# Optimization experiments

Hardware: AMD Instinct MI355X
Metric: run time of the kernel (lower is better)

The kernel has to match this reference:

```python
import jax, jax.numpy as jnp
import numpy as np

N_NODES = 50000
N_EDGES = 800000
NUM_IN, NUM_HID, NUM_OUT = 512, 256, 64
EPS = 1e-12


def agnn_conv(x, src, dst, beta, num_nodes):
    # PyG AGNNConv: score(j->i) = beta * cos(x_i, x_j); softmax over incoming
    # edges of each target node i; out_i = sum_j alpha_ij * x_j.
    norm = jnp.maximum(jnp.linalg.norm(x, axis=1, keepdims=True), EPS)
    xn = x / norm                                      # [N, H]
    scores = beta * jnp.sum(xn[dst] * xn[src], axis=1)  # [E]
    m = jax.ops.segment_max(scores, dst, num_segments=num_nodes)
    e = jnp.exp(scores - m[dst])
    s = jax.ops.segment_sum(e, dst, num_segments=num_nodes)
    alpha = e / s[dst]                                  # [E]
    return jax.ops.segment_sum(alpha[:, None] * x[src], dst, num_segments=num_nodes)


def setup_inputs() -> dict:
    key = jax.random.key(0)
    ks = jax.random.split(key, 7)
    x = jax.random.normal(ks[0], (N_NODES, NUM_IN), dtype=jnp.float32)
    edge_index = jax.random.randint(ks[1], (2, N_EDGES), 0, N_NODES, dtype=jnp.int64)
    w1 = jax.random.normal(ks[2], (NUM_HID, NUM_IN), dtype=jnp.float32) / np.sqrt(NUM_IN)
    b1 = jnp.zeros((NUM_HID,), dtype=jnp.float32)
    beta2 = jnp.ones((1,), dtype=jnp.float32)
    w2 = jax.random.normal(ks[3], (NUM_OUT, NUM_HID), dtype=jnp.float32) / np.sqrt(NUM_HID)
    b2 = jnp.zeros((NUM_OUT,), dtype=jnp.float32)
    return {"x": x, "edge_index": edge_index, "w1": w1, "b1": b1,
            "beta2": beta2, "w2": w2, "b2": b2}


def reference(x, edge_index, w1, b1, beta2, w2, b2):
    n = x.shape[0]
    # add self-loops (PyG AGNNConv default add_self_loops=True)
    loops = jnp.arange(n, dtype=edge_index.dtype)
    src = jnp.concatenate([edge_index[0], loops])
    dst = jnp.concatenate([edge_index[1], loops])

    h = jax.nn.relu(x @ w1.T + b1)                       # [N, H] (eval: dropout = id)
    h = agnn_conv(h, src, dst, jnp.float32(1.0), n)      # prop1, fixed beta=1
    z1 = h
    h = agnn_conv(h, src, dst, beta2[0], n)              # prop2, learnable beta
    z2 = h
    logits = h @ w2.T + b2                               # [N, C]
    return (z1, z2, jax.nn.log_softmax(logits, axis=1))
```

## Files before the change

kernel.cpp:

```cpp
#include <hip/hip_runtime.h>

#define N_NODES 50000
#define N_EDGES 800000
#define ETOT (N_EDGES + N_NODES)
#define DIN 512
#define HID 256
#define NOUT 64
#define SCAN_CHUNK 2048

typedef __attribute__((ext_vector_type(8))) short short8;
typedef __attribute__((ext_vector_type(4))) float f32x4;
typedef __attribute__((ext_vector_type(4))) unsigned short us4;

__device__ __forceinline__ unsigned short f2bf(float f) {
  union { float f; unsigned u; } x; x.f = f;
  unsigned r = x.u + 0x7fff + ((x.u >> 16) & 1);
  return (unsigned short)(r >> 16);
}
__device__ __forceinline__ float bf2f(unsigned short b) {
  return __uint_as_float(((unsigned)b) << 16);
}

__device__ __forceinline__ int edge_at(const void* ei, long long idx, int is32) {
  if (is32) return ((const int*)ei)[idx];
  return (int)((const long long*)ei)[idx];
}

__global__ void initK(const void* ei, int* cursor, int* flag) {
  int i = blockIdx.x * blockDim.x + threadIdx.x;
  if (i < N_NODES) cursor[i] = 1;
  if (blockIdx.x == 0 && threadIdx.x < 64) {
    int lane = threadIdx.x;
    bool bad = false;
#pragma unroll
    for (int j = 0; j < 32; ++j) {
      long long v = ((const long long*)ei)[lane * 32 + j];
      bad |= (v < 0 || v >= N_NODES);
    }
    bool anybad = __any(bad);
    if (lane == 0) *flag = anybad ? 1 : 0;
  }
}

__global__ void histK(const void* ei, const int* flag, int* cursor) {
  int e = blockIdx.x * blockDim.x + threadIdx.x;
  if (e >= N_EDGES) return;
  int f = *flag;
  int d = edge_at(ei, (long long)N_EDGES + e, f);
  atomicAdd(&cursor[d], 1);
}

__global__ void scan1K(const int* counts, int* excl, int* bsums) {
  __shared__ int sdata[256];
  int base = blockIdx.x * SCAN_CHUNK;
  int t = threadIdx.x;
  int local[8];
  int sum = 0;
#pragma unroll
  for (int j = 0; j < 8; ++j) {
    int idx = base + t * 8 + j;
    int v = (idx < N_NODES) ? counts[idx] : 0;
    local[j] = sum;
    sum += v;
  }
  sdata[t] = sum;
  __syncthreads();
  for (int off = 1; off < 256; off <<= 1) {
    int v = (t >= off) ? sdata[t - off] : 0;
    __syncthreads();
    sdata[t] += v;
    __syncthreads();
  }
  int texcl = (t == 0) ? 0 : sdata[t - 1];
#pragma unroll
  for (int j = 0; j < 8; ++j) {
    int idx = base + t * 8 + j;
    if (idx < N_NODES) excl[idx] = texcl + local[j];
  }
  if (t == 255) bsums[blockIdx.x] = sdata[255];
}

__global__ void scan2K(int* bsums, int nb) {
  if (threadIdx.x == 0 && blockIdx.x == 0) {
    int run = 0;
    for (int i = 0; i < nb; ++i) { int v = bsums[i]; bsums[i] = run; run += v; }
  }
}

__global__ void scan3K(int* row_ptr, const int* bsums, int* cursor) {
  int i = blockIdx.x * blockDim.x + threadIdx.x;
  if (i < N_NODES) {
    int v = row_ptr[i] + bsums[i >> 11];
    row_ptr[i] = v;
    cursor[i] = v;
    if (i == 0) row_ptr[N_NODES] = ETOT;
  }
}

__global__ void scatterK(const void* ei, const int* flag, int* cursor, int* col) {
  int e = blockIdx.x * blockDim.x + threadIdx.x;
  if (e < N_EDGES) {
    int f = *flag;
    int s = edge_at(ei, e, f);
    int d = edge_at(ei, (long long)N_EDGES + e, f);
    int pos = atomicAdd(&cursor[d], 1);
    col[pos] = s;
  } else if (e < N_EDGES + N_NODES) {
    int i = e - N_EDGES;
    int pos = atomicAdd(&cursor[i], 1);
    col[pos] = i;
  }
}

__global__ __launch_bounds__(256) void gemm1MF(const float* __restrict__ A,
                                               const float* __restrict__ W,
                                               const float* __restrict__ bias,
                                               unsigned short* __restrict__ C) {
  __shared__ short As[128 * 64];
  __shared__ short Bs[128 * 64];
  int t = threadIdx.x;
  int w = t >> 6, lane = t & 63;
  int wr = w >> 1, wc = w & 1;
  int row0 = blockIdx.x * 128;
  int col0 = blockIdx.y * 128;
  f32x4 acc[4][4];
#pragma unroll
  for (int mi = 0; mi < 4; ++mi)
#pragma unroll
    for (int ni = 0; ni < 4; ++ni) acc[mi][ni] = (f32x4){0.f, 0.f, 0.f, 0.f};

  for (int k0 = 0; k0 < DIN; k0 += 64) {
#pragma unroll
    for (int it = 0; it < 4; ++it) {
      int si = it * 256 + t;
      int r = si >> 3, g = si & 7;
      int slot = g ^ (r & 7);
      int gr = row0 + r;
      gr = (gr < N_NODES) ? gr : (N_NODES - 1);
      const float* pa = &A[(long long)gr * DIN + k0 + g * 8];
      float4 a0 = *(const float4*)pa;
      float4 a1 = *(const float4*)(pa + 4);
      short8 sa;
      sa[0] = f2bf(a0.x); sa[1] = f2bf(a0.y); sa[2] = f2bf(a0.z); sa[3] = f2bf(a0.w);
      sa[4] = f2bf(a1.x); sa[5] = f2bf(a1.y); sa[6] = f2bf(a1.z); sa[7] = f2bf(a1.w);
      *(short8*)&As[(r * 8 + slot) * 8] = sa;
      const float* pb = &W[(long long)(col0 + r) * DIN + k0 + g * 8];
      float4 b0 = *(const float4*)pb;
      float4 b1v = *(const float4*)(pb + 4);
      short8 sb;
      sb[0] = f2bf(b0.x); sb[1] = f2bf(b0.y); sb[2] = f2bf(b0.z); sb[3] = f2bf(b0.w);
      sb[4] = f2bf(b1v.x); sb[5] = f2bf(b1v.y); sb[6] = f2bf(b1v.z); sb[7] = f2bf(b1v.w);
      *(short8*)&Bs[(r * 8 + slot) * 8] = sb;
    }
    __syncthreads();
#pragma unroll
    for (int kk = 0; kk < 2; ++kk) {
      int g = kk * 4 + (lane >> 4);
      short8 af[4], bfr[4];
#pragma unroll
      for (int mi = 0; mi < 4; ++mi) {
        int r = wr * 64 + mi * 16 + (lane & 15);
        af[mi] = *(const short8*)&As[(r * 8 + (g ^ (r & 7))) * 8];
      }
#pragma unroll
      for (int ni = 0; ni < 4; ++ni) {
        int c = wc * 64 + ni * 16 + (lane & 15);
        bfr[ni] = *(const short8*)&Bs[(c * 8 + (g ^ (c & 7))) * 8];
      }
#pragma unroll
      for (int mi = 0; mi < 4; ++mi)
#pragma unroll
        for (int ni = 0; ni < 4; ++ni)
          acc[mi][ni] = __builtin_amdgcn_mfma_f32_16x16x32_bf16(af[mi], bfr[ni], acc[mi][ni], 0, 0, 0);
    }
    __syncthreads();
  }

  int fr = lane & 15, fq = lane >> 4;
#pragma unroll
  for (int ni = 0; ni < 4; ++ni) {
    int colv = col0 + wc * 64 + ni * 16 + fr;
    float bv = bias[colv];
#pragma unroll
    for (int mi = 0; mi < 4; ++mi) {
#pragma unroll
      for (int j = 0; j < 4; ++j) {
        int row = row0 + wr * 64 + mi * 16 + fq * 4 + j;
        if (row < N_NODES)
          C[(long long)row * HID + colv] = f2bf(fmaxf(acc[mi][ni][j] + bv, 0.f));
      }
    }
  }
}

__global__ __launch_bounds__(256) void normBF(const unsigned short* __restrict__ hb,
                                              float* __restrict__ invn) {
  int w = (blockIdx.x * 256 + threadIdx.x) >> 6;
  int lane = threadIdx.x & 63;
  if (w >= N_NODES) return;
  us4 v = *(const us4*)&hb[(long long)w * HID + lane * 4];
  float x = bf2f(v.x), y = bf2f(v.y), z = bf2f(v.z), ww = bf2f(v.w);
  float s = x * x + y * y + z * z + ww * ww;
#pragma unroll
  for (int off = 32; off >= 1; off >>= 1) s += __shfl_xor(s, off);
  if (lane == 0) invn[w] = 1.0f / fmaxf(sqrtf(s), 1e-12f);
}

__global__ __launch_bounds__(256) void convK(const unsigned short* __restrict__ hb,
                                             const float* __restrict__ invn,
                                             const int* __restrict__ row_ptr,
                                             const int* __restrict__ col,
                                             const float* __restrict__ beta_ptr,
                                             float* __restrict__ hout,
                                             unsigned short* __restrict__ hout_bf) {
  int w = (blockIdx.x * 256 + threadIdx.x) >> 6;
  int lane = threadIdx.x & 63;
  if (w >= N_NODES) return;
  int g = lane >> 4;
  int sub = lane & 15;
  float beta = beta_ptr ? beta_ptr[0] : 1.0f;
  float babs = fabsf(beta);

  const unsigned short* hrow = &hb[(long long)w * HID + sub * 16];
  short8 hia = *(const short8*)hrow;
  short8 hib = *(const short8*)(hrow + 8);
  float hi[16];
#pragma unroll
  for (int q = 0; q < 8; ++q) {
    hi[q] = bf2f((unsigned short)hia[q]);
    hi[8 + q] = bf2f((unsigned short)hib[q]);
  }
  float scale_i = invn[w] * beta;

  int e0 = row_ptr[w], e1 = row_ptr[w + 1];
  int nit = (e1 - e0 + 3) >> 2;
  float Z = 0.f;
  float acc[16];
#pragma unroll
  for (int q = 0; q < 16; ++q) acc[q] = 0.f;

  for (int it = 0; it < nit; ++it) {
    int ee = e0 + it * 4 + g;
    bool valid = ee < e1;
    int s = col[valid ? ee : (e1 - 1)];
    float is = invn[s];
    const unsigned short* hj = &hb[(long long)s * HID + sub * 16];
    short8 ja = *(const short8*)hj;
    short8 jb = *(const short8*)(hj + 8);
    float hjf[16];
#pragma unroll
    for (int q = 0; q < 8; ++q) {
      hjf[q] = bf2f((unsigned short)ja[q]);
      hjf[8 + q] = bf2f((unsigned short)jb[q]);
    }
    float p = 0.f;
#pragma unroll
    for (int q = 0; q < 16; ++q) p += hi[q] * hjf[q];
    p += __shfl_xor(p, 1);
    p += __shfl_xor(p, 2);
    p += __shfl_xor(p, 4);
    p += __shfl_xor(p, 8);
    float sc = p * scale_i * is;
    float wt = valid ? __expf(sc - babs) : 0.f;
    Z += wt;
#pragma unroll
    for (int q = 0; q < 16; ++q) acc[q] += wt * hjf[q];
  }

#pragma unroll
  for (int q = 0; q < 16; ++q) {
    acc[q] += __shfl_xor(acc[q], 16);
    acc[q] += __shfl_xor(acc[q], 32);
  }
  Z += __shfl_xor(Z, 16);
  Z += __shfl_xor(Z, 32);
  float r = 1.0f / Z;

  if (g == 0) {
    float* po = &hout[(long long)w * HID + sub * 16];
#pragma unroll
    for (int q4 = 0; q4 < 4; ++q4) {
      float4 o;
      o.x = acc[q4 * 4 + 0] * r;
      o.y = acc[q4 * 4 + 1] * r;
      o.z = acc[q4 * 4 + 2] * r;
      o.w = acc[q4 * 4 + 3] * r;
      *(float4*)&po[q4 * 4] = o;
    }
  } else if (g == 1 && hout_bf) {
    unsigned short* pb = &hout_bf[(long long)w * HID + sub * 16];
#pragma unroll
    for (int q4 = 0; q4 < 4; ++q4) {
      us4 ob;
      ob.x = f2bf(acc[q4 * 4 + 0] * r);
      ob.y = f2bf(acc[q4 * 4 + 1] * r);
      ob.z = f2bf(acc[q4 * 4 + 2] * r);
      ob.w = f2bf(acc[q4 * 4 + 3] * r);
      *(us4*)&pb[q4 * 4] = ob;
    }
  }
}

__global__ __launch_bounds__(256) void headK2(const float* __restrict__ Z,
                                              const float* __restrict__ W,
                                              const float* __restrict__ bias,
                                              float* __restrict__ out) {
  __shared__ float smem[2 * 32 * 68];
  float* As = smem;
  float* Bs = smem + 32 * 68;
  int t = threadIdx.x;
  int tx = t & 15, ty = t >> 4;
  int row0 = blockIdx.x * 64;
  float acc[4][4] = {};
  int lr = t >> 3;
  int lc4 = t & 7;

  for (int k0 = 0; k0 < HID; k0 += 32) {
#pragma unroll
    for (int rr = 0; rr < 64; rr += 32) {
      int gr = row0 + lr + rr;
      float4 va = (gr < N_NODES)
                      ? *(const float4*)&Z[(long long)gr * HID + k0 + lc4 * 4]
                      : make_float4(0.f, 0.f, 0.f, 0.f);
      As[(lc4 * 4 + 0) * 68 + lr + rr] = va.x;
      As[(lc4 * 4 + 1) * 68 + lr + rr] = va.y;
      As[(lc4 * 4 + 2) * 68 + lr + rr] = va.z;
      As[(lc4 * 4 + 3) * 68 + lr + rr] = va.w;
      int gc = lr + rr;
      float4 vb = *(const float4*)&W[(long long)gc * HID + k0 + lc4 * 4];
      Bs[(lc4 * 4 + 0) * 68 + lr + rr] = vb.x;
      Bs[(lc4 * 4 + 1) * 68 + lr + rr] = vb.y;
      Bs[(lc4 * 4 + 2) * 68 + lr + rr] = vb.z;
      Bs[(lc4 * 4 + 3) * 68 + lr + rr] = vb.w;
    }
    __syncthreads();
#pragma unroll
    for (int kk = 0; kk < 32; ++kk) {
      float4 a4 = *(const float4*)&As[kk * 68 + ty * 4];
      float4 b4 = *(const float4*)&Bs[kk * 68 + tx * 4];
      acc[0][0] += a4.x * b4.x; acc[0][1] += a4.x * b4.y; acc[0][2] += a4.x * b4.z; acc[0][3] += a4.x * b4.w;
      acc[1][0] += a4.y * b4.x; acc[1][1] += a4.y * b4.y; acc[1][2] += a4.y * b4.z; acc[1][3] += a4.y * b4.w;
      acc[2][0] += a4.z * b4.x; acc[2][1] += a4.z * b4.y; acc[2][2] += a4.z * b4.z; acc[2][3] += a4.z * b4.w;
      acc[3][0] += a4.w * b4.x; acc[3][1] += a4.w * b4.y; acc[3][2] += a4.w * b4.z; acc[3][3] += a4.w * b4.w;
    }
    __syncthreads();
  }

  float* ls = smem;
  float4 bv = *(const float4*)&bias[tx * 4];
#pragma unroll
  for (int r = 0; r < 4; ++r) {
    int lrow = ty * 4 + r;
    ls[lrow * 65 + tx * 4 + 0] = acc[r][0] + bv.x;
    ls[lrow * 65 + tx * 4 + 1] = acc[r][1] + bv.y;
    ls[lrow * 65 + tx * 4 + 2] = acc[r][2] + bv.z;
    ls[lrow * 65 + tx * 4 + 3] = acc[r][3] + bv.w;
  }
  __syncthreads();

  int wid = t >> 6, lane = t & 63;
#pragma unroll
  for (int rr2 = wid; rr2 < 64; rr2 += 4) {
    int node = row0 + rr2;
    if (node < N_NODES) {
      float v = ls[rr2 * 65 + lane];
      float mx = v;
#pragma unroll
      for (int off = 32; off >= 1; off >>= 1) mx = fmaxf(mx, __shfl_xor(mx, off));
      float ex = __expf(v - mx);
      float se = ex;
#pragma unroll
      for (int off = 32; off >= 1; off >>= 1) se += __shfl_xor(se, off);
      out[(long long)node * NOUT + lane] = v - mx - __logf(se);
    }
  }
}

extern "C" void kernel_launch(void* const* d_in, const int* in_sizes, int n_in,
                              void* d_out, int out_size, void* d_ws, size_t ws_size,
                              hipStream_t stream) {
  (void)in_sizes; (void)n_in; (void)out_size; (void)ws_size;
  const float* x = (const float*)d_in[0];
  const void* ei = d_in[1];
  const float* w1 = (const float*)d_in[2];
  const float* b1 = (const float*)d_in[3];
  const float* beta2 = (const float*)d_in[4];
  const float* w2 = (const float*)d_in[5];
  const float* b2 = (const float*)d_in[6];

  float* z1 = (float*)d_out;
  float* z2 = z1 + (size_t)N_NODES * HID;
  float* lsm = z2 + (size_t)N_NODES * HID;

  unsigned short* h_bf = (unsigned short*)d_ws;
  unsigned short* z1_bf = h_bf + (size_t)N_NODES * HID;
  float* invn = (float*)(z1_bf + (size_t)N_NODES * HID);
  int* row_ptr = (int*)(invn + N_NODES);
  int* cursor = row_ptr + N_NODES + 1;
  int* colv = cursor + N_NODES;
  int* bsums = colv + ETOT;
  int* flag = bsums + 64;

  int nScan = (N_NODES + SCAN_CHUNK - 1) / SCAN_CHUNK;

  initK<<<(N_NODES + 255) / 256, 256, 0, stream>>>(ei, cursor, flag);

  dim3 gg((N_NODES + 127) / 128, HID / 128);
  gemm1MF<<<gg, 256, 0, stream>>>(x, w1, b1, h_bf);

  histK<<<(N_EDGES + 255) / 256, 256, 0, stream>>>(ei, flag, cursor);
  scan1K<<<nScan, 256, 0, stream>>>(cursor, row_ptr, bsums);
  scan2K<<<1, 64, 0, stream>>>(bsums, nScan);
  scan3K<<<(N_NODES + 255) / 256, 256, 0, stream>>>(row_ptr, bsums, cursor);
  scatterK<<<(N_EDGES + N_NODES + 255) / 256, 256, 0, stream>>>(ei, flag, cursor, colv);

  normBF<<<(N_NODES + 3) / 4, 256, 0, stream>>>(h_bf, invn);
  convK<<<(N_NODES + 3) / 4, 256, 0, stream>>>(h_bf, invn, row_ptr, colv, nullptr, z1, z1_bf);
  normBF<<<(N_NODES + 3) / 4, 256, 0, stream>>>(z1_bf, invn);
  convK<<<(N_NODES + 3) / 4, 256, 0, stream>>>(z1_bf, invn, row_ptr, colv, beta2, z2, nullptr);

  headK2<<<(N_NODES + 63) / 64, 256, 0, stream>>>(z2, w2, b2, lsm);
}
```

Before: 363.3 us.

## Double-buffer GEMM1 LDS tiles with register prefetch of next K slice

```diff
diff --git a/kernel.cpp b/kernel.cpp
--- a/kernel.cpp
+++ b/kernel.cpp
@@ -116,67 +116,92 @@
                                                const float* __restrict__ W,
                                                const float* __restrict__ bias,
                                                unsigned short* __restrict__ C) {
-  __shared__ short As[128 * 64];
-  __shared__ short Bs[128 * 64];
+  __shared__ short As[2][128 * 32];
+  __shared__ short Bs[2][128 * 32];
   int t = threadIdx.x;
   int w = t >> 6, lane = t & 63;
   int wr = w >> 1, wc = w & 1;
   int row0 = blockIdx.x * 128;
   int col0 = blockIdx.y * 128;
+
+  int sr = t >> 1, sh = t & 1;
+  int gra = row0 + sr;
+  if (gra >= N_NODES) gra = N_NODES - 1;
+  const float* pa_base = &A[(long long)gra * DIN + sh * 16];
+  const float* pb_base = &W[(long long)(col0 + sr) * DIN + sh * 16];
+  int q = (sr >> 1) & 3;
+  int slot0 = sr * 32 + (((sh << 1) + 0) ^ q) * 8;
+  int slot1 = sr * 32 + (((sh << 1) + 1) ^ q) * 8;
+
   f32x4 acc[4][4];
 #pragma unroll
   for (int mi = 0; mi < 4; ++mi)
 #pragma unroll
     for (int ni = 0; ni < 4; ++ni) acc[mi][ni] = (f32x4){0.f, 0.f, 0.f, 0.f};
 
-  for (int k0 = 0; k0 < DIN; k0 += 64) {
-#pragma unroll
-    for (int it = 0; it < 4; ++it) {
-      int si = it * 256 + t;
-      int r = si >> 3, g = si & 7;
-      int slot = g ^ (r & 7);
-      int gr = row0 + r;
-      gr = (gr < N_NODES) ? gr : (N_NODES - 1);
-      const float* pa = &A[(long long)gr * DIN + k0 + g * 8];
-      float4 a0 = *(const float4*)pa;
-      float4 a1 = *(const float4*)(pa + 4);
-      short8 sa;
-      sa[0] = f2bf(a0.x); sa[1] = f2bf(a0.y); sa[2] = f2bf(a0.z); sa[3] = f2bf(a0.w);
-      sa[4] = f2bf(a1.x); sa[5] = f2bf(a1.y); sa[6] = f2bf(a1.z); sa[7] = f2bf(a1.w);
-      *(short8*)&As[(r * 8 + slot) * 8] = sa;
-      const float* pb = &W[(long long)(col0 + r) * DIN + k0 + g * 8];
-      float4 b0 = *(const float4*)pb;
-      float4 b1v = *(const float4*)(pb + 4);
-      short8 sb;
-      sb[0] = f2bf(b0.x); sb[1] = f2bf(b0.y); sb[2] = f2bf(b0.z); sb[3] = f2bf(b0.w);
-      sb[4] = f2bf(b1v.x); sb[5] = f2bf(b1v.y); sb[6] = f2bf(b1v.z); sb[7] = f2bf(b1v.w);
-      *(short8*)&Bs[(r * 8 + slot) * 8] = sb;
-    }
+  float4 a0, a1, a2, a3, b0, b1, b2, b3;
+
+#define LOADREGS(k0)                                   \
+  do {                                                 \
+    const float4* pa = (const float4*)(pa_base + (k0)); \
+    const float4* pb = (const float4*)(pb_base + (k0)); \
+    a0 = pa[0]; a1 = pa[1]; a2 = pa[2]; a3 = pa[3];    \
+    b0 = pb[0]; b1 = pb[1]; b2 = pb[2]; b3 = pb[3];    \
+  } while (0)
+
+#define CVT_WRITE(buf)                                                      \
+  do {                                                                      \
+    short8 s;                                                               \
+    s[0] = f2bf(a0.x); s[1] = f2bf(a0.y); s[2] = f2bf(a0.z); s[3] = f2bf(a0.w); \
+    s[4] = f2bf(a1.x); s[5] = f2bf(a1.y); s[6] = f2bf(a1.z); s[7] = f2bf(a1.w); \
+    *(short8*)&As[buf][slot0] = s;                                          \
+    s[0] = f2bf(a2.x); s[1] = f2bf(a2.y); s[2] = f2bf(a2.z); s[3] = f2bf(a2.w); \
+    s[4] = f2bf(a3.x); s[5] = f2bf(a3.y); s[6] = f2bf(a3.z); s[7] = f2bf(a3.w); \
+    *(short8*)&As[buf][slot1] = s;                                          \
+    s[0] = f2bf(b0.x); s[1] = f2bf(b0.y); s[2] = f2bf(b0.z); s[3] = f2bf(b0.w); \
+    s[4] = f2bf(b1.x); s[5] = f2bf(b1.y); s[6] = f2bf(b1.z); s[7] = f2bf(b1.w); \
+    *(short8*)&Bs[buf][slot0] = s;                                          \
+    s[0] = f2bf(b2.x); s[1] = f2bf(b2.y); s[2] = f2bf(b2.z); s[3] = f2bf(b2.w); \
+    s[4] = f2bf(b3.x); s[5] = f2bf(b3.y); s[6] = f2bf(b3.z); s[7] = f2bf(b3.w); \
+    *(short8*)&Bs[buf][slot1] = s;                                          \
+  } while (0)
+
+  LOADREGS(0);
+  CVT_WRITE(0);
+  __syncthreads();
+
+  int g = lane >> 4;
+  int fr = lane & 15;
+
+#pragma unroll
+  for (int ks = 0; ks < 16; ++ks) {
+    int cur = ks & 1;
+    if (ks < 15) LOADREGS((ks + 1) * 32);
+
+    short8 af[4], bfr[4];
+#pragma unroll
+    for (int mi = 0; mi < 4; ++mi) {
+      int r = wr * 64 + mi * 16 + fr;
+      af[mi] = *(const short8*)&As[cur][r * 32 + ((g ^ ((r >> 1) & 3)) * 8)];
+    }
+#pragma unroll
+    for (int ni = 0; ni < 4; ++ni) {
+      int c = wc * 64 + ni * 16 + fr;
+      bfr[ni] = *(const short8*)&Bs[cur][c * 32 + ((g ^ ((c >> 1) & 3)) * 8)];
+    }
+#pragma unroll
+    for (int mi = 0; mi < 4; ++mi)
+#pragma unroll
+      for (int ni = 0; ni < 4; ++ni)
+        acc[mi][ni] = __builtin_amdgcn_mfma_f32_16x16x32_bf16(af[mi], bfr[ni], acc[mi][ni], 0, 0, 0);
+
+    if (ks < 15) CVT_WRITE(cur ^ 1);
     __syncthreads();
-#pragma unroll
-    for (int kk = 0; kk < 2; ++kk) {
-      int g = kk * 4 + (lane >> 4);
-      short8 af[4], bfr[4];
-#pragma unroll
-      for (int mi = 0; mi < 4; ++mi) {
-        int r = wr * 64 + mi * 16 + (lane & 15);
-        af[mi] = *(const short8*)&As[(r * 8 + (g ^ (r & 7))) * 8];
-      }
-#pragma unroll
-      for (int ni = 0; ni < 4; ++ni) {
-        int c = wc * 64 + ni * 16 + (lane & 15);
-        bfr[ni] = *(const short8*)&Bs[(c * 8 + (g ^ (c & 7))) * 8];
-      }
-#pragma unroll
-      for (int mi = 0; mi < 4; ++mi)
-#pragma unroll
-        for (int ni = 0; ni < 4; ++ni)
-          acc[mi][ni] = __builtin_amdgcn_mfma_f32_16x16x32_bf16(af[mi], bfr[ni], acc[mi][ni], 0, 0, 0);
-    }
-    __syncthreads();
-  }
-
-  int fr = lane & 15, fq = lane >> 4;
+  }
+#undef LOADREGS
+#undef CVT_WRITE
+
+  int fq = lane >> 4;
 #pragma unroll
   for (int ni = 0; ni < 4; ++ni) {
     int colv = col0 + wc * 64 + ni * 16 + fr;
```

Result: slower. 371.4 us (+2.2%).

## Pre-convert x and w1 to bf16 and stream GEMM tiles via global_load_lds

Applied to the files above, without the earlier changes.

```diff
diff --git a/kernel.cpp b/kernel.cpp
--- a/kernel.cpp
+++ b/kernel.cpp
@@ -20,6 +20,9 @@
 __device__ __forceinline__ float bf2f(unsigned short b) {
   return __uint_as_float(((unsigned)b) << 16);
 }
+
+#define AS1(p) ((const __attribute__((address_space(1))) unsigned int*)(p))
+#define AS3(p) ((__attribute__((address_space(3))) unsigned int*)(p))
 
 __device__ __forceinline__ int edge_at(const void* ei, long long idx, int is32) {
   if (is32) return ((const int*)ei)[idx];
@@ -112,60 +115,82 @@
   }
 }
 
-__global__ __launch_bounds__(256) void gemm1MF(const float* __restrict__ A,
-                                               const float* __restrict__ W,
+__global__ __launch_bounds__(256) void cvtK(const float* __restrict__ x,
+                                            const float* __restrict__ w1,
+                                            unsigned short* __restrict__ xb,
+                                            unsigned short* __restrict__ wb) {
+  const long long NX = (long long)N_NODES * DIN / 8;
+  const long long NW = (long long)HID * DIN / 8;
+  long long stride = (long long)gridDim.x * blockDim.x;
+  for (long long c = (long long)blockIdx.x * blockDim.x + threadIdx.x;
+       c < NX + NW; c += stride) {
+    const float* src;
+    unsigned short* dst;
+    if (c < NX) { src = x + c * 8; dst = xb + c * 8; }
+    else { src = w1 + (c - NX) * 8; dst = wb + (c - NX) * 8; }
+    float4 v0 = ((const float4*)src)[0];
+    float4 v1 = ((const float4*)src)[1];
+    short8 s;
+    s[0] = f2bf(v0.x); s[1] = f2bf(v0.y); s[2] = f2bf(v0.z); s[3] = f2bf(v0.w);
+    s[4] = f2bf(v1.x); s[5] = f2bf(v1.y); s[6] = f2bf(v1.z); s[7] = f2bf(v1.w);
+    *(short8*)dst = s;
+  }
+}
+
+__global__ __launch_bounds__(256) void gemm1MF(const unsigned short* __restrict__ Ab,
+                                               const unsigned short* __restrict__ Bb,
                                                const float* __restrict__ bias,
                                                unsigned short* __restrict__ C) {
   __shared__ short As[128 * 64];
   __shared__ short Bs[128 * 64];
   int t = threadIdx.x;
-  int w = t >> 6, lane = t & 63;
-  int wr = w >> 1, wc = w & 1;
+  int wv = t >> 6, ln = t & 63;
+  int wr = wv >> 1, wc = wv & 1;
   int row0 = blockIdx.x * 128;
   int col0 = blockIdx.y * 128;
+
+  int lr = ln >> 3, lc = ln & 7;
+  int scol = ((lc ^ lr) << 3);
+
+  int ar0 = row0 + lr;
+  const unsigned short* bbase = &Bb[(long long)(col0 + lr) * DIN + scol];
+
   f32x4 acc[4][4];
 #pragma unroll
   for (int mi = 0; mi < 4; ++mi)
 #pragma unroll
     for (int ni = 0; ni < 4; ++ni) acc[mi][ni] = (f32x4){0.f, 0.f, 0.f, 0.f};
 
+  int g = ln >> 4;
+  int fr = ln & 15;
+
   for (int k0 = 0; k0 < DIN; k0 += 64) {
 #pragma unroll
     for (int it = 0; it < 4; ++it) {
-      int si = it * 256 + t;
-      int r = si >> 3, g = si & 7;
-      int slot = g ^ (r & 7);
-      int gr = row0 + r;
-      gr = (gr < N_NODES) ? gr : (N_NODES - 1);
-      const float* pa = &A[(long long)gr * DIN + k0 + g * 8];
-      float4 a0 = *(const float4*)pa;
-      float4 a1 = *(const float4*)(pa + 4);
-      short8 sa;
-      sa[0] = f2bf(a0.x); sa[1] = f2bf(a0.y); sa[2] = f2bf(a0.z); sa[3] = f2bf(a0.w);
-      sa[4] = f2bf(a1.x); sa[5] = f2bf(a1.y); sa[6] = f2bf(a1.z); sa[7] = f2bf(a1.w);
-      *(short8*)&As[(r * 8 + slot) * 8] = sa;
-      const float* pb = &W[(long long)(col0 + r) * DIN + k0 + g * 8];
-      float4 b0 = *(const float4*)pb;
-      float4 b1v = *(const float4*)(pb + 4);
-      short8 sb;
-      sb[0] = f2bf(b0.x); sb[1] = f2bf(b0.y); sb[2] = f2bf(b0.z); sb[3] = f2bf(b0.w);
-      sb[4] = f2bf(b1v.x); sb[5] = f2bf(b1v.y); sb[6] = f2bf(b1v.z); sb[7] = f2bf(b1v.w);
-      *(short8*)&Bs[(r * 8 + slot) * 8] = sb;
-    }
-    __syncthreads();
+      int chunk = it * 4 + wv;
+      int ar = ar0 + chunk * 8;
+      if (ar >= N_NODES) ar = N_NODES - 1;
+      const unsigned short* asrc = &Ab[(long long)ar * DIN + k0 + scol];
+      __builtin_amdgcn_global_load_lds(AS1(asrc), AS3(&As[chunk * 512]), 16, 0, 0);
+      const unsigned short* bsrc = bbase + k0 + (long long)chunk * 8 * DIN;
+      __builtin_amdgcn_global_load_lds(AS1(bsrc), AS3(&Bs[chunk * 512]), 16, 0, 0);
+    }
+    __syncthreads();
+
 #pragma unroll
     for (int kk = 0; kk < 2; ++kk) {
-      int g = kk * 4 + (lane >> 4);
       short8 af[4], bfr[4];
 #pragma unroll
       for (int mi = 0; mi < 4; ++mi) {
-        int r = wr * 64 + mi * 16 + (lane & 15);
-        af[mi] = *(const short8*)&As[(r * 8 + (g ^ (r & 7))) * 8];
+        int r = wr * 64 + mi * 16 + fr;
+        int slot = (kk * 4 + g) ^ (r & 7);
+        af[mi] = *(const short8*)&As[r * 64 + slot * 8];
       }
 #pragma unroll
       for (int ni = 0; ni < 4; ++ni) {
-        int c = wc * 64 + ni * 16 + (lane & 15);
-        bfr[ni] = *(const short8*)&Bs[(c * 8 + (g ^ (c & 7))) * 8];
+        int c = wc * 64 + ni * 16 + fr;
+        int slot = (kk * 4 + g) ^ (c & 7);
+        bfr[ni] = *(const short8*)&Bs[c * 64 + slot * 8];
       }
 #pragma unroll
       for (int mi = 0; mi < 4; ++mi)
@@ -176,7 +201,7 @@
     __syncthreads();
   }
 
-  int fr = lane & 15, fq = lane >> 4;
+  int fq = ln >> 4;
 #pragma unroll
   for (int ni = 0; ni < 4; ++ni) {
     int colv = col0 + wc * 64 + ni * 16 + fr;
@@ -400,13 +425,17 @@
   int* colv = cursor + N_NODES;
   int* bsums = colv + ETOT;
   int* flag = bsums + 64;
+  unsigned short* wb = (unsigned short*)(flag + 4);
+
+  unsigned short* xb = (unsigned short*)z2;
 
   int nScan = (N_NODES + SCAN_CHUNK - 1) / SCAN_CHUNK;
 
+  cvtK<<<2048, 256, 0, stream>>>(x, w1, xb, wb);
   initK<<<(N_NODES + 255) / 256, 256, 0, stream>>>(ei, cursor, flag);
 
   dim3 gg((N_NODES + 127) / 128, HID / 128);
-  gemm1MF<<<gg, 256, 0, stream>>>(x, w1, b1, h_bf);
+  gemm1MF<<<gg, 256, 0, stream>>>(xb, wb, b1, h_bf);
 
   histK<<<(N_EDGES + 255) / 256, 256, 0, stream>>>(ei, flag, cursor);
   scan1K<<<nScan, 256, 0, stream>>>(cursor, row_ptr, bsums);
```

New measurement: 364.0 us. No clear change (+0.2%).
